# Kernel tuning notes

Measured on AMD Instinct MI355X. Metric: run time of the kernel, lower is better.

Reference implementation:

```python
import jax, jax.numpy as jnp
import numpy as np

N_AGENTS = 8192
OBS_DIM = 520
EMBED = 64
HID = 128
N_ACT = 6


def setup_inputs() -> dict:
    key = jax.random.key(0)
    ks = jax.random.split(key, 16)
    s = 0.05  # small init scale for numerical stability
    return {
        "obs": jax.random.normal(ks[0], (N_AGENTS, OBS_DIM), jnp.float32),
        "beliefs": jax.random.normal(ks[1], (N_AGENTS, HID), jnp.float32),
        "W1": jax.random.normal(ks[2], (OBS_DIM, EMBED), jnp.float32) * s,
        "b1": jnp.zeros((EMBED,), jnp.float32),
        "W2": jax.random.normal(ks[3], (EMBED, EMBED), jnp.float32) * s,
        "b2": jnp.zeros((EMBED,), jnp.float32),
        "Wb": jax.random.normal(ks[4], (HID, EMBED), jnp.float32) * s,
        "bb": jnp.zeros((EMBED,), jnp.float32),
        "Wg": jax.random.normal(ks[5], (2 * EMBED, HID), jnp.float32) * s,
        "bg": jnp.zeros((HID,), jnp.float32),
        "Wir": jax.random.normal(ks[6], (HID, HID), jnp.float32) * s,
        "Wiz": jax.random.normal(ks[7], (HID, HID), jnp.float32) * s,
        "Win": jax.random.normal(ks[8], (HID, HID), jnp.float32) * s,
        "Whr": jax.random.normal(ks[9], (HID, HID), jnp.float32) * s,
        "bhr": jnp.zeros((HID,), jnp.float32),
        "Whz": jax.random.normal(ks[10], (HID, HID), jnp.float32) * s,
        "bhz": jnp.zeros((HID,), jnp.float32),
        "Whn": jax.random.normal(ks[11], (HID, HID), jnp.float32) * s,
        "bhn": jnp.zeros((HID,), jnp.float32),
        "Wout": jax.random.normal(ks[12], (HID, N_ACT), jnp.float32) * s,
        "bout": jnp.zeros((N_ACT,), jnp.float32),
    }


def reference(obs, beliefs, W1, b1, W2, b2, Wb, bb, Wg, bg,
              Wir, Wiz, Win, Whr, bhr, Whz, bhz, Whn, bhn, Wout, bout):
    n_agents = obs.shape[0]
    # obs MLP: Dense -> relu -> Dense -> relu  [A, EMBED]
    h_obs = jax.nn.relu(obs @ W1 + b1)
    h_obs = jax.nn.relu(h_obs @ W2 + b2)
    # belief projection [A, EMBED]
    bp = beliefs @ Wb + bb
    # self-attention over beliefs with diagonal masked out
    attn_logits = (bp @ bp.T) / jnp.sqrt(jnp.asarray(EMBED, bp.dtype))
    attn_logits = attn_logits + jnp.eye(n_agents, dtype=bp.dtype) * (-1e8)
    attn_weights = jax.nn.softmax(attn_logits, axis=-1)
    contexts = attn_weights @ bp  # [A, EMBED]
    # GRU input projection [A, HID]
    gru_in = jnp.concatenate([h_obs, contexts], axis=-1) @ Wg + bg
    # flax GRUCell (input denses bias-free, hidden denses biased)
    r = jax.nn.sigmoid(gru_in @ Wir + beliefs @ Whr + bhr)
    z = jax.nn.sigmoid(gru_in @ Wiz + beliefs @ Whz + bhz)
    n = jnp.tanh(gru_in @ Win + r * (beliefs @ Whn + bhn))
    new_beliefs = (1.0 - z) * n + z * beliefs
    logits = new_beliefs @ Wout + bout
    return (logits, new_beliefs)
```

## Files before the change

### kernel.cpp

```cpp
#include <hip/hip_runtime.h>

#define A_N 8192
#define OBS_D 520
#define EMB 64
#define HID 128
#define NACT 6
#define SPLIT 16

typedef short bf16x8 __attribute__((ext_vector_type(8)));
typedef _Float16 half8 __attribute__((ext_vector_type(8)));
typedef float f32x4 __attribute__((ext_vector_type(4)));
typedef unsigned short u16;
typedef unsigned int u32;

#define MFMA_BF(a,b,c) __builtin_amdgcn_mfma_f32_16x16x32_bf16(a,b,c,0,0,0)
#define MFMA_FH(a,b,c) __builtin_amdgcn_mfma_f32_16x16x32_f16(a,b,c,0,0,0)

__device__ inline u32 fbits(float f){ union{float f; u32 u;}v; v.f=f; return v.u; }
__device__ inline float fval(u32 u){ union{u32 u; float f;}v; v.u=u; return v.f; }
__device__ inline u16 f2bf(float f){ u32 u=fbits(f); u += 0x7fffu + ((u>>16)&1u); return (u16)(u>>16); }
__device__ inline u32 pk_bf(float pe, float po){
  return __builtin_amdgcn_perm(fbits(po), fbits(pe), 0x07060302u);
}
__device__ inline float sigmoidf_fast(float x){
  x = fminf(fmaxf(x, -30.f), 30.f);
  return 1.f / (1.f + __expf(-x));
}
__device__ inline float tanhf_fast(float x){
  x = fminf(fmaxf(x, -15.f), 15.f);
  float e = __expf(-2.f*x);
  return (1.f - e) / (1.f + e);
}

#define EXP2C 0.18033688011112042f

__global__ __launch_bounds__(256) void kPrep(
    const float* __restrict__ Wg, const float* __restrict__ Wir,
    const float* __restrict__ Wiz, const float* __restrict__ Win,
    const float* __restrict__ Whr, const float* __restrict__ Whz,
    const float* __restrict__ Whn, const float* __restrict__ W1,
    const float* __restrict__ W2, const float* __restrict__ Wb,
    _Float16* __restrict__ WT, _Float16* __restrict__ W1T,
    _Float16* __restrict__ W2T, u16* __restrict__ WbT)
{
  __shared__ float tile[64][65];
  const int t = threadIdx.x, b = blockIdx.x;

  const float* src; int k0, c0, srcStride, kValid;
  if (b < 28) {
    const int mi = b >> 2, tl = b & 3;
    src = mi==0?Wg: mi==1?Wir: mi==2?Wiz: mi==3?Win: mi==4?Whr: mi==5?Whz: Whn;
    k0 = (tl >> 1) * 64; c0 = (tl & 1) * 64; srcStride = 128; kValid = 128;
  } else if (b < 37) {
    src = W1; k0 = (b - 28) * 64; c0 = 0; srcStride = 64; kValid = OBS_D;
  } else if (b < 38) {
    src = W2; k0 = 0; c0 = 0; srcStride = 64; kValid = 64;
  } else {
    src = Wb; k0 = (b - 38) * 64; c0 = 0; srcStride = 64; kValid = 128;
  }
  #pragma unroll
  for (int i = 0; i < 16; i++) {
    const int idx = i * 256 + t;
    const int rr = idx >> 6, cc = idx & 63;
    tile[rr][cc] = (k0 + rr < kValid) ? src[(size_t)(k0 + rr) * srcStride + c0 + cc] : 0.f;
  }
  __syncthreads();
  if (b < 28) {
    const int mi = b >> 2;
    _Float16* dst = WT + (size_t)mi * 16384;
    #pragma unroll
    for (int i = 0; i < 16; i++) {
      const int idx = i * 256 + t;
      const int rr = idx >> 6, cc = idx & 63;
      dst[(size_t)(c0 + rr) * 128 + k0 + cc] = (_Float16)tile[cc][rr];
    }
  } else if (b < 37) {
    #pragma unroll
    for (int i = 0; i < 16; i++) {
      const int idx = i * 256 + t;
      const int rr = idx >> 6, cc = idx & 63;
      if (k0 + cc < 544)
        W1T[(size_t)rr * 544 + k0 + cc] = (_Float16)tile[cc][rr];
    }
  } else if (b < 38) {
    #pragma unroll
    for (int i = 0; i < 16; i++) {
      const int idx = i * 256 + t;
      const int rr = idx >> 6, cc = idx & 63;
      W2T[(size_t)rr * 64 + cc] = (_Float16)tile[cc][rr];
    }
  } else {
    #pragma unroll
    for (int i = 0; i < 16; i++) {
      const int idx = i * 256 + t;
      const int rr = idx >> 6, cc = idx & 63;
      WbT[(size_t)rr * 128 + k0 + cc] = f2bf(tile[cc][rr]);
    }
  }
}

__global__ __launch_bounds__(256) void kA2(
    const float* __restrict__ beliefs, const u16* __restrict__ WbT,
    const float* __restrict__ bb, u16* __restrict__ bp, u16* __restrict__ bpT)
{
  const int lane = threadIdx.x & 63, wid = threadIdx.x >> 6;
  const int m = lane & 15, quad = lane >> 4;
  const int r0 = blockIdx.x * 64 + wid * 16;
  f32x4 c[4];
  #pragma unroll
  for (int ct = 0; ct < 4; ct++) c[ct] = (f32x4){0.f,0.f,0.f,0.f};

  #pragma unroll
  for (int s = 0; s < 4; s++) {
    const int k0 = s*32;
    const float* ap = beliefs + (size_t)(r0+m)*HID + k0 + quad*8;
    float4 a0 = *(const float4*)ap;
    float4 a1 = *(const float4*)(ap + 4);
    union { u16 e[8]; bf16x8 v; } av;
    av.e[0]=f2bf(a0.x); av.e[1]=f2bf(a0.y); av.e[2]=f2bf(a0.z); av.e[3]=f2bf(a0.w);
    av.e[4]=f2bf(a1.x); av.e[5]=f2bf(a1.y); av.e[6]=f2bf(a1.z); av.e[7]=f2bf(a1.w);
    #pragma unroll
    for (int ct = 0; ct < 4; ct++) {
      bf16x8 bw = *(const bf16x8*)(WbT + (size_t)(ct*16+m)*128 + k0 + quad*8);
      c[ct] = MFMA_BF(av.v, bw, c[ct]);
    }
  }
  #pragma unroll
  for (int ct = 0; ct < 4; ct++) {
    const int col = ct*16 + m;
    const float bbv = bb[col];
    u16 e[4];
    #pragma unroll
    for (int r = 0; r < 4; r++) e[r] = f2bf(c[ct][r] + bbv);
    #pragma unroll
    for (int r = 0; r < 4; r++)
      bp[(size_t)(r0 + quad*4 + r)*EMB + col] = e[r];
    uint2 pkv;
    pkv.x = (u32)e[0] | ((u32)e[1] << 16);
    pkv.y = (u32)e[2] | ((u32)e[3] << 16);
    *(uint2*)(bpT + (size_t)col*A_N + r0 + quad*4) = pkv;
  }
}

__global__ __launch_bounds__(256) void kM(
    const u16* __restrict__ bp, const u16* __restrict__ bpT,
    u16* __restrict__ ctxp, float* __restrict__ sums,
    const float* __restrict__ obs, const _Float16* __restrict__ W1T,
    const float* __restrict__ b1, const _Float16* __restrict__ W2T,
    const float* __restrict__ b2, _Float16* __restrict__ h2f)
{
  __shared__ __align__(16) u16 P[4][4][16 * 72];
  const int lane = threadIdx.x & 63;
  const int wid  = threadIdx.x >> 6;
  const int m = lane & 15, quad = lane >> 4;

  if (blockIdx.x >= 128) {
    const int w = (blockIdx.x - 128) * 4 + wid;
    const int split = w >> 7;
    const int qt = w & 127;
    const int q0 = qt * 64;

    bf16x8 qa[4][2];
    #pragma unroll
    for (int f = 0; f < 4; f++) {
      const u16* qr = bp + (size_t)(q0 + f*16 + m)*EMB + quad*8;
      qa[f][0] = *(const bf16x8*)(qr);
      qa[f][1] = *(const bf16x8*)(qr + 32);
    }
    f32x4 oacc[4][4];
    #pragma unroll
    for (int f = 0; f < 4; f++)
      #pragma unroll
      for (int d = 0; d < 4; d++) oacc[f][d] = (f32x4){0.f,0.f,0.f,0.f};
    float rowsum[4] = {0.f, 0.f, 0.f, 0.f};

    const int kbeg = split * (A_N / SPLIT);
    const int kend = kbeg + (A_N / SPLIT);

    for (int k0 = kbeg; k0 < kend; k0 += 64) {
      #pragma unroll
      for (int jt = 0; jt < 4; jt++) {
        const u16* kr = bp + (size_t)(k0 + jt*16 + m)*EMB + quad*8;
        const bf16x8 kb0 = *(const bf16x8*)(kr);
        const bf16x8 kb1 = *(const bf16x8*)(kr + 32);
        #pragma unroll
        for (int f = 0; f < 4; f++) {
          f32x4 s = (f32x4){0.f,0.f,0.f,0.f};
          s = MFMA_BF(kb0, qa[f][0], s);
          s = MFMA_BF(kb1, qa[f][1], s);
          float p0 = __builtin_amdgcn_exp2f(s[0]*EXP2C);
          float p1 = __builtin_amdgcn_exp2f(s[1]*EXP2C);
          float p2 = __builtin_amdgcn_exp2f(s[2]*EXP2C);
          float p3 = __builtin_amdgcn_exp2f(s[3]*EXP2C);
          if ((k0 + jt*16) == (q0 + f*16)) {
            const int jl = quad*4;
            if (jl + 0 == m) p0 = 0.f;
            if (jl + 1 == m) p1 = 0.f;
            if (jl + 2 == m) p2 = 0.f;
            if (jl + 3 == m) p3 = 0.f;
          }
          rowsum[f] += (p0 + p1) + (p2 + p3);
          uint2 pkv; pkv.x = pk_bf(p0, p1); pkv.y = pk_bf(p2, p3);
          *(uint2*)&P[wid][f][m*72 + jt*16 + quad*4] = pkv;
        }
      }
      bf16x8 vb[4][2];
      #pragma unroll
      for (int dtt = 0; dtt < 4; dtt++) {
        const u16* vr = bpT + (size_t)(dtt*16+m)*A_N + k0 + quad*8;
        vb[dtt][0] = *(const bf16x8*)(vr);
        vb[dtt][1] = *(const bf16x8*)(vr + 32);
      }
      asm volatile("s_waitcnt lgkmcnt(0)" ::: "memory");
      #pragma unroll
      for (int f = 0; f < 4; f++) {
        const bf16x8 pa0 = *(const bf16x8*)&P[wid][f][m*72 + quad*8];
        const bf16x8 pa1 = *(const bf16x8*)&P[wid][f][m*72 + 32 + quad*8];
        #pragma unroll
        for (int dtt = 0; dtt < 4; dtt++) {
          oacc[f][dtt] = MFMA_BF(pa0, vb[dtt][0], oacc[f][dtt]);
          oacc[f][dtt] = MFMA_BF(pa1, vb[dtt][1], oacc[f][dtt]);
        }
      }
    }

    #pragma unroll
    for (int f = 0; f < 4; f++) {
      float v = rowsum[f];
      v += __shfl_xor(v, 16, 64);
      v += __shfl_xor(v, 32, 64);
      if (lane < 16)
        sums[(size_t)split*A_N + q0 + f*16 + lane] = v;
    }
    #pragma unroll
    for (int f = 0; f < 4; f++) {
      const size_t base = ((size_t)split*A_N + q0 + f*16) * EMB;
      #pragma unroll
      for (int dtt = 0; dtt < 4; dtt++)
        #pragma unroll
        for (int r = 0; r < 4; r++)
          ctxp[base + (size_t)(quad*4+r)*EMB + dtt*16 + m] = f2bf(oacc[f][dtt][r]);
    }
  } else {
    const int r0 = blockIdx.x * 64 + wid * 16;
    f32x4 oa[4];
    #pragma unroll
    for (int ct = 0; ct < 4; ct++) oa[ct] = (f32x4){0.f,0.f,0.f,0.f};

    for (int s = 0; s < 17; s++) {
      const int k0 = s * 32;
      union { _Float16 e[8]; half8 v; } af;
      if (s < 16) {
        const float* ap = obs + (size_t)(r0+m)*OBS_D + k0 + quad*8;
        float4 a0 = *(const float4*)ap;
        float4 a1 = *(const float4*)(ap + 4);
        af.e[0]=(_Float16)a0.x; af.e[1]=(_Float16)a0.y; af.e[2]=(_Float16)a0.z; af.e[3]=(_Float16)a0.w;
        af.e[4]=(_Float16)a1.x; af.e[5]=(_Float16)a1.y; af.e[6]=(_Float16)a1.z; af.e[7]=(_Float16)a1.w;
      } else {
        #pragma unroll
        for (int j = 0; j < 8; j++) af.e[j] = (_Float16)0.f;
        if (quad == 0) {
          const float* ap = obs + (size_t)(r0+m)*OBS_D + 512;
          float4 a0 = *(const float4*)ap;
          float4 a1 = *(const float4*)(ap + 4);
          af.e[0]=(_Float16)a0.x; af.e[1]=(_Float16)a0.y; af.e[2]=(_Float16)a0.z; af.e[3]=(_Float16)a0.w;
          af.e[4]=(_Float16)a1.x; af.e[5]=(_Float16)a1.y; af.e[6]=(_Float16)a1.z; af.e[7]=(_Float16)a1.w;
        }
      }
      #pragma unroll
      for (int ct = 0; ct < 4; ct++) {
        half8 bw = *(const half8*)(W1T + (size_t)(ct*16+m)*544 + k0 + quad*8);
        oa[ct] = MFMA_FH(af.v, bw, oa[ct]);
      }
    }
    _Float16* H1 = (_Float16*)&P[wid][0][0];
    #pragma unroll
    for (int ct = 0; ct < 4; ct++) {
      const float b1v = b1[ct*16 + m];
      #pragma unroll
      for (int r = 0; r < 4; r++) {
        float v = fmaxf(oa[ct][r] + b1v, 0.f);
        H1[(quad*4+r)*72 + ct*16 + m] = (_Float16)v;
      }
    }
    __syncthreads();
    f32x4 ob[4];
    #pragma unroll
    for (int ct = 0; ct < 4; ct++) ob[ct] = (f32x4){0.f,0.f,0.f,0.f};
    #pragma unroll
    for (int s2 = 0; s2 < 2; s2++) {
      half8 ah = *(const half8*)(H1 + m*72 + s2*32 + quad*8);
      #pragma unroll
      for (int ct = 0; ct < 4; ct++) {
        half8 bw = *(const half8*)(W2T + (size_t)(ct*16+m)*64 + s2*32 + quad*8);
        ob[ct] = MFMA_FH(ah, bw, ob[ct]);
      }
    }
    #pragma unroll
    for (int ct = 0; ct < 4; ct++) {
      const float b2v = b2[ct*16 + m];
      #pragma unroll
      for (int r = 0; r < 4; r++) {
        float v = fmaxf(ob[ct][r] + b2v, 0.f);
        h2f[(size_t)(r0 + quad*4 + r)*EMB + ct*16 + m] = (_Float16)v;
      }
    }
  }
}

__global__ __launch_bounds__(256) void kRed(
    const u16* __restrict__ ctxp, const float* __restrict__ sums,
    _Float16* __restrict__ xh)
{
  const int idx = blockIdx.x * 256 + threadIdx.x;
  const int row = idx >> 5;
  const int cp  = idx & 31;
  float s0 = 0.f, s1 = 0.f, ss = 0.f;
  #pragma unroll
  for (int sp = 0; sp < SPLIT; sp++) {
    const u32 u = *(const u32*)(ctxp + ((size_t)sp*A_N + row)*EMB + cp*2);
    s0 += fval(u << 16);
    s1 += fval(u & 0xffff0000u);
    ss += sums[(size_t)sp*A_N + row];
  }
  const float inv = 1.f / ss;
  union { _Float16 e[2]; u32 u; } o;
  o.e[0] = (_Float16)(s0 * inv);
  o.e[1] = (_Float16)(s1 * inv);
  *(u32*)(xh + (size_t)row*EMB + cp*2) = o.u;
}

__global__ __launch_bounds__(256) void k3_gru(
    const float* __restrict__ beliefs, const _Float16* __restrict__ h2f,
    const _Float16* __restrict__ xh,
    const _Float16* __restrict__ WT,
    const float* __restrict__ bg, const float* __restrict__ bhr,
    const float* __restrict__ bhz, const float* __restrict__ bhn,
    const float* __restrict__ Wout, const float* __restrict__ bout,
    float* __restrict__ out)
{
  __shared__ _Float16 xf[16][136];
  __shared__ _Float16 belf[16][136];
  __shared__ _Float16 gruf[16][136];
  const int t = threadIdx.x;
  const int lane = t & 63, wid = t >> 6;
  const int m = lane & 15, quad = lane >> 4;
  const int r0 = blockIdx.x * 16;

  {
    const int row = t >> 4, seg = t & 15;
    const float* bpR = beliefs + (size_t)(r0+row)*HID + seg*8;
    float4 a0 = *(const float4*)bpR;
    float4 a1 = *(const float4*)(bpR + 4);
    union { _Float16 e[8]; half8 v; } hb;
    hb.e[0]=(_Float16)a0.x; hb.e[1]=(_Float16)a0.y; hb.e[2]=(_Float16)a0.z; hb.e[3]=(_Float16)a0.w;
    hb.e[4]=(_Float16)a1.x; hb.e[5]=(_Float16)a1.y; hb.e[6]=(_Float16)a1.z; hb.e[7]=(_Float16)a1.w;
    *(half8*)&belf[row][seg*8] = hb.v;
  }
  if (t < 128) {
    const int crow = t >> 3, cdg = t & 7;
    half8 hv = *(const half8*)(h2f + (size_t)(r0+crow)*EMB + cdg*8);
    *(half8*)&xf[crow][cdg*8] = hv;
    half8 xv = *(const half8*)(xh + (size_t)(r0+crow)*EMB + cdg*8);
    *(half8*)&xf[crow][64 + cdg*8] = xv;
  }
  __syncthreads();

  f32x4 g[2];
  g[0] = (f32x4){0.f,0.f,0.f,0.f}; g[1] = (f32x4){0.f,0.f,0.f,0.f};
  #pragma unroll
  for (int s = 0; s < 4; s++) {
    half8 ax = *(const half8*)&xf[m][s*32 + quad*8];
    #pragma unroll
    for (int ci = 0; ci < 2; ci++) {
      const int ct = wid*2 + ci;
      half8 bw = *(const half8*)(WT + (size_t)(ct*16+m)*128 + s*32 + quad*8);
      g[ci] = MFMA_FH(ax, bw, g[ci]);
    }
  }
  #pragma unroll
  for (int ci = 0; ci < 2; ci++) {
    const int col = (wid*2+ci)*16 + m;
    const float bgv = bg[col];
    #pragma unroll
    for (int r = 0; r < 4; r++)
      gruf[quad*4+r][col] = (_Float16)(g[ci][r] + bgv);
  }
  __syncthreads();

  f32x4 RV[2], ZV[2];
  #pragma unroll
  for (int gidx = 0; gidx < 3; gidx++) {
    const _Float16* WiTg = WT + (size_t)(1+gidx)*16384;
    const _Float16* WhTg = WT + (size_t)(4+gidx)*16384;
    f32x4 gi[2], gh[2];
    gi[0]=(f32x4){0.f,0.f,0.f,0.f}; gi[1]=(f32x4){0.f,0.f,0.f,0.f};
    gh[0]=(f32x4){0.f,0.f,0.f,0.f}; gh[1]=(f32x4){0.f,0.f,0.f,0.f};
    #pragma unroll
    for (int s = 0; s < 4; s++) {
      half8 ag = *(const half8*)&gruf[m][s*32 + quad*8];
      half8 ab = *(const half8*)&belf[m][s*32 + quad*8];
      #pragma unroll
      for (int ci = 0; ci < 2; ci++) {
        const int ct = wid*2 + ci;
        half8 bi = *(const half8*)(WiTg + (size_t)(ct*16+m)*128 + s*32 + quad*8);
        half8 bh = *(const half8*)(WhTg + (size_t)(ct*16+m)*128 + s*32 + quad*8);
        gi[ci] = MFMA_FH(ag, bi, gi[ci]);
        gh[ci] = MFMA_FH(ab, bh, gh[ci]);
      }
    }
    if (gidx == 0) {
      #pragma unroll
      for (int ci = 0; ci < 2; ci++) {
        const float bv = bhr[(wid*2+ci)*16 + m];
        #pragma unroll
        for (int r = 0; r < 4; r++) RV[ci][r] = sigmoidf_fast(gi[ci][r] + gh[ci][r] + bv);
      }
    } else if (gidx == 1) {
      #pragma unroll
      for (int ci = 0; ci < 2; ci++) {
        const float bv = bhz[(wid*2+ci)*16 + m];
        #pragma unroll
        for (int r = 0; r < 4; r++) ZV[ci][r] = sigmoidf_fast(gi[ci][r] + gh[ci][r] + bv);
      }
    } else {
      #pragma unroll
      for (int ci = 0; ci < 2; ci++) {
        const int col = (wid*2+ci)*16 + m;
        const float bv = bhn[col];
        #pragma unroll
        for (int r = 0; r < 4; r++) {
          const int row = quad*4 + r;
          float bel = beliefs[(size_t)(r0+row)*HID + col];
          float pre = gi[ci][r] + RV[ci][r] * (gh[ci][r] + bv);
          float nv = tanhf_fast(pre);
          float nb = (1.f - ZV[ci][r]) * nv + ZV[ci][r] * bel;
          out[(size_t)NACT*A_N + (size_t)(r0+row)*HID + col] = nb;
          xf[row][col] = (_Float16)nb;
        }
      }
    }
  }
  __syncthreads();

  if (t < 16*NACT) {
    const int row = t / NACT, c = t % NACT;
    float a = bout[c];
    #pragma unroll 8
    for (int k = 0; k < HID; k++)
      a += (float)xf[row][k] * Wout[(size_t)k*NACT + c];
    out[(size_t)(r0+row)*NACT + c] = a;
  }
}

extern "C" void kernel_launch(void* const* d_in, const int* in_sizes, int n_in,
                              void* d_out, int out_size, void* d_ws, size_t ws_size,
                              hipStream_t stream) {
  const float* obs     = (const float*)d_in[0];
  const float* beliefs = (const float*)d_in[1];
  const float* W1      = (const float*)d_in[2];
  const float* b1      = (const float*)d_in[3];
  const float* W2      = (const float*)d_in[4];
  const float* b2      = (const float*)d_in[5];
  const float* Wb      = (const float*)d_in[6];
  const float* bb      = (const float*)d_in[7];
  const float* Wg      = (const float*)d_in[8];
  const float* bg      = (const float*)d_in[9];
  const float* Wir     = (const float*)d_in[10];
  const float* Wiz     = (const float*)d_in[11];
  const float* Win     = (const float*)d_in[12];
  const float* Whr     = (const float*)d_in[13];
  const float* bhr     = (const float*)d_in[14];
  const float* Whz     = (const float*)d_in[15];
  const float* bhz     = (const float*)d_in[16];
  const float* Whn     = (const float*)d_in[17];
  const float* bhn     = (const float*)d_in[18];
  const float* Wout    = (const float*)d_in[19];
  const float* bout    = (const float*)d_in[20];
  float* out = (float*)d_out;

  char* ws = (char*)d_ws;
  _Float16* h2f  = (_Float16*)(ws);
  u16*      bp   = (u16*)(ws + 1048576);
  u16*      bpT  = (u16*)(ws + 2097152);
  u16*      ctxp = (u16*)(ws + 3145728);
  float*    sums = (float*)(ws + 19922944);
  _Float16* WT   = (_Float16*)(ws + 20447232);
  _Float16* W1T  = (_Float16*)(ws + 20676608);
  _Float16* W2T  = (_Float16*)(ws + 20746240);
  u16*      WbT  = (u16*)(ws + 20754432);
  _Float16* xh   = (_Float16*)(ws + 1048576);

  hipLaunchKernelGGL(kPrep, dim3(40), dim3(256), 0, stream,
                     Wg, Wir, Wiz, Win, Whr, Whz, Whn, W1, W2, Wb, WT, W1T, W2T, WbT);
  hipLaunchKernelGGL(kA2, dim3(128), dim3(256), 0, stream, beliefs, WbT, bb, bp, bpT);
  hipLaunchKernelGGL(kM, dim3(128 + (A_N / 64) * SPLIT / 4), dim3(256), 0, stream,
                     bp, bpT, ctxp, sums, obs, W1T, b1, W2T, b2, h2f);
  hipLaunchKernelGGL(kRed, dim3(1024), dim3(256), 0, stream, ctxp, sums, xh);
  hipLaunchKernelGGL(k3_gru, dim3(512), dim3(256), 0, stream,
                     beliefs, h2f, xh, WT, bg, bhr, bhz, bhn, Wout, bout, out);
}
```

Before: 187.4 us.

## Fuse belief projection into prep kernel, reorder kM blocks, double GRU rows per block

Merges the Wb transpose and belief projection kernel into the weight-prep kernel: each projection block converts Wb to bf16 in LDS itself, so one launch and the WbT global round trip go away. In kM the attention blocks now come first in the grid and the obs-MLP blocks after them, so the long attention work is scheduled earlier. The GRU kernel processes 32 rows per block instead of 16, reusing each loaded weight fragment for two MFMA row tiles and halving the grid. In exchange, every projection block redoes the Wb conversion, and the GRU kernel uses more LDS and registers with fewer blocks.

```diff
diff --git a/kernel.cpp b/kernel.cpp
--- a/kernel.cpp
+++ b/kernel.cpp
@@ -34,111 +34,111 @@
 
 #define EXP2C 0.18033688011112042f
 
-__global__ __launch_bounds__(256) void kPrep(
+__global__ __launch_bounds__(256) void kPrep2(
     const float* __restrict__ Wg, const float* __restrict__ Wir,
     const float* __restrict__ Wiz, const float* __restrict__ Win,
     const float* __restrict__ Whr, const float* __restrict__ Whz,
     const float* __restrict__ Whn, const float* __restrict__ W1,
     const float* __restrict__ W2, const float* __restrict__ Wb,
+    const float* __restrict__ beliefs, const float* __restrict__ bb,
     _Float16* __restrict__ WT, _Float16* __restrict__ W1T,
-    _Float16* __restrict__ W2T, u16* __restrict__ WbT)
+    _Float16* __restrict__ W2T, u16* __restrict__ bp, u16* __restrict__ bpT)
 {
   __shared__ float tile[64][65];
+  __shared__ u16 WbL[64][136];
   const int t = threadIdx.x, b = blockIdx.x;
 
-  const float* src; int k0, c0, srcStride, kValid;
-  if (b < 28) {
-    const int mi = b >> 2, tl = b & 3;
-    src = mi==0?Wg: mi==1?Wir: mi==2?Wiz: mi==3?Win: mi==4?Whr: mi==5?Whz: Whn;
-    k0 = (tl >> 1) * 64; c0 = (tl & 1) * 64; srcStride = 128; kValid = 128;
-  } else if (b < 37) {
-    src = W1; k0 = (b - 28) * 64; c0 = 0; srcStride = 64; kValid = OBS_D;
-  } else if (b < 38) {
-    src = W2; k0 = 0; c0 = 0; srcStride = 64; kValid = 64;
-  } else {
-    src = Wb; k0 = (b - 38) * 64; c0 = 0; srcStride = 64; kValid = 128;
-  }
-  #pragma unroll
-  for (int i = 0; i < 16; i++) {
-    const int idx = i * 256 + t;
-    const int rr = idx >> 6, cc = idx & 63;
-    tile[rr][cc] = (k0 + rr < kValid) ? src[(size_t)(k0 + rr) * srcStride + c0 + cc] : 0.f;
-  }
-  __syncthreads();
-  if (b < 28) {
-    const int mi = b >> 2;
-    _Float16* dst = WT + (size_t)mi * 16384;
+  if (b < 38) {
+    const float* src; int k0, c0, srcStride, kValid;
+    if (b < 28) {
+      const int mi = b >> 2, tl = b & 3;
+      src = mi==0?Wg: mi==1?Wir: mi==2?Wiz: mi==3?Win: mi==4?Whr: mi==5?Whz: Whn;
+      k0 = (tl >> 1) * 64; c0 = (tl & 1) * 64; srcStride = 128; kValid = 128;
+    } else if (b < 37) {
+      src = W1; k0 = (b - 28) * 64; c0 = 0; srcStride = 64; kValid = OBS_D;
+    } else {
+      src = W2; k0 = 0; c0 = 0; srcStride = 64; kValid = 64;
+    }
     #pragma unroll
     for (int i = 0; i < 16; i++) {
       const int idx = i * 256 + t;
       const int rr = idx >> 6, cc = idx & 63;
-      dst[(size_t)(c0 + rr) * 128 + k0 + cc] = (_Float16)tile[cc][rr];
-    }
-  } else if (b < 37) {
-    #pragma unroll
-    for (int i = 0; i < 16; i++) {
-      const int idx = i * 256 + t;
-      const int rr = idx >> 6, cc = idx & 63;
-      if (k0 + cc < 544)
-        W1T[(size_t)rr * 544 + k0 + cc] = (_Float16)tile[cc][rr];
-    }
-  } else if (b < 38) {
-    #pragma unroll
-    for (int i = 0; i < 16; i++) {
-      const int idx = i * 256 + t;
-      const int rr = idx >> 6, cc = idx & 63;
-      W2T[(size_t)rr * 64 + cc] = (_Float16)tile[cc][rr];
+      tile[rr][cc] = (k0 + rr < kValid) ? src[(size_t)(k0 + rr) * srcStride + c0 + cc] : 0.f;
+    }
+    __syncthreads();
+    if (b < 28) {
+      const int mi = b >> 2;
+      _Float16* dst = WT + (size_t)mi * 16384;
+      #pragma unroll
+      for (int i = 0; i < 16; i++) {
+        const int idx = i * 256 + t;
+        const int rr = idx >> 6, cc = idx & 63;
+        dst[(size_t)(c0 + rr) * 128 + k0 + cc] = (_Float16)tile[cc][rr];
+      }
+    } else if (b < 37) {
+      #pragma unroll
+      for (int i = 0; i < 16; i++) {
+        const int idx = i * 256 + t;
+        const int rr = idx >> 6, cc = idx & 63;
+        if (k0 + cc < 544)
+          W1T[(size_t)rr * 544 + k0 + cc] = (_Float16)tile[cc][rr];
+      }
+    } else {
+      #pragma unroll
+      for (int i = 0; i < 16; i++) {
+        const int idx = i * 256 + t;
+        const int rr = idx >> 6, cc = idx & 63;
+        W2T[(size_t)rr * 64 + cc] = (_Float16)tile[cc][rr];
+      }
     }
   } else {
-    #pragma unroll
-    for (int i = 0; i < 16; i++) {
-      const int idx = i * 256 + t;
-      const int rr = idx >> 6, cc = idx & 63;
-      WbT[(size_t)rr * 128 + k0 + cc] = f2bf(tile[cc][rr]);
-    }
-  }
-}
-
-__global__ __launch_bounds__(256) void kA2(
-    const float* __restrict__ beliefs, const u16* __restrict__ WbT,
-    const float* __restrict__ bb, u16* __restrict__ bp, u16* __restrict__ bpT)
-{
-  const int lane = threadIdx.x & 63, wid = threadIdx.x >> 6;
-  const int m = lane & 15, quad = lane >> 4;
-  const int r0 = blockIdx.x * 64 + wid * 16;
-  f32x4 c[4];
-  #pragma unroll
-  for (int ct = 0; ct < 4; ct++) c[ct] = (f32x4){0.f,0.f,0.f,0.f};
-
-  #pragma unroll
-  for (int s = 0; s < 4; s++) {
-    const int k0 = s*32;
-    const float* ap = beliefs + (size_t)(r0+m)*HID + k0 + quad*8;
-    float4 a0 = *(const float4*)ap;
-    float4 a1 = *(const float4*)(ap + 4);
-    union { u16 e[8]; bf16x8 v; } av;
-    av.e[0]=f2bf(a0.x); av.e[1]=f2bf(a0.y); av.e[2]=f2bf(a0.z); av.e[3]=f2bf(a0.w);
-    av.e[4]=f2bf(a1.x); av.e[5]=f2bf(a1.y); av.e[6]=f2bf(a1.z); av.e[7]=f2bf(a1.w);
+    const int lane = t & 63, wid = t >> 6;
+    const int m = lane & 15, quad = lane >> 4;
+    const int r0 = (b - 38) * 64 + wid * 16;
+
+    #pragma unroll
+    for (int i = 0; i < 8; i++) {
+      const int i4 = i * 256 + t;
+      float4 w4 = ((const float4*)Wb)[i4];
+      const int k = i4 >> 4, c = (i4 & 15) * 4;
+      WbL[c+0][k] = f2bf(w4.x); WbL[c+1][k] = f2bf(w4.y);
+      WbL[c+2][k] = f2bf(w4.z); WbL[c+3][k] = f2bf(w4.w);
+    }
+    __syncthreads();
+
+    f32x4 acc[4];
+    #pragma unroll
+    for (int ct = 0; ct < 4; ct++) acc[ct] = (f32x4){0.f,0.f,0.f,0.f};
+    #pragma unroll
+    for (int s = 0; s < 4; s++) {
+      const int k0 = s*32;
+      const float* ap = beliefs + (size_t)(r0+m)*HID + k0 + quad*8;
+      float4 a0 = *(const float4*)ap;
+      float4 a1 = *(const float4*)(ap + 4);
+      union { u16 e[8]; bf16x8 v; } av;
+      av.e[0]=f2bf(a0.x); av.e[1]=f2bf(a0.y); av.e[2]=f2bf(a0.z); av.e[3]=f2bf(a0.w);
+      av.e[4]=f2bf(a1.x); av.e[5]=f2bf(a1.y); av.e[6]=f2bf(a1.z); av.e[7]=f2bf(a1.w);
+      #pragma unroll
+      for (int ct = 0; ct < 4; ct++) {
+        bf16x8 bw = *(const bf16x8*)&WbL[ct*16+m][k0 + quad*8];
+        acc[ct] = MFMA_BF(av.v, bw, acc[ct]);
+      }
+    }
     #pragma unroll
     for (int ct = 0; ct < 4; ct++) {
-      bf16x8 bw = *(const bf16x8*)(WbT + (size_t)(ct*16+m)*128 + k0 + quad*8);
-      c[ct] = MFMA_BF(av.v, bw, c[ct]);
-    }
-  }
-  #pragma unroll
-  for (int ct = 0; ct < 4; ct++) {
-    const int col = ct*16 + m;
-    const float bbv = bb[col];
-    u16 e[4];
-    #pragma unroll
-    for (int r = 0; r < 4; r++) e[r] = f2bf(c[ct][r] + bbv);
-    #pragma unroll
-    for (int r = 0; r < 4; r++)
-      bp[(size_t)(r0 + quad*4 + r)*EMB + col] = e[r];
-    uint2 pkv;
-    pkv.x = (u32)e[0] | ((u32)e[1] << 16);
-    pkv.y = (u32)e[2] | ((u32)e[3] << 16);
-    *(uint2*)(bpT + (size_t)col*A_N + r0 + quad*4) = pkv;
+      const int col = ct*16 + m;
+      const float bbv = bb[col];
+      u16 e[4];
+      #pragma unroll
+      for (int r = 0; r < 4; r++) e[r] = f2bf(acc[ct][r] + bbv);
+      #pragma unroll
+      for (int r = 0; r < 4; r++)
+        bp[(size_t)(r0 + quad*4 + r)*EMB + col] = e[r];
+      uint2 pkv;
+      pkv.x = (u32)e[0] | ((u32)e[1] << 16);
+      pkv.y = (u32)e[2] | ((u32)e[3] << 16);
+      *(uint2*)(bpT + (size_t)col*A_N + r0 + quad*4) = pkv;
+    }
   }
 }
 
@@ -154,8 +154,8 @@
   const int wid  = threadIdx.x >> 6;
   const int m = lane & 15, quad = lane >> 4;
 
-  if (blockIdx.x >= 128) {
-    const int w = (blockIdx.x - 128) * 4 + wid;
+  if (blockIdx.x < 512) {
+    const int w = blockIdx.x * 4 + wid;
     const int split = w >> 7;
     const int qt = w & 127;
     const int q0 = qt * 64;
@@ -242,7 +242,7 @@
           ctxp[base + (size_t)(quad*4+r)*EMB + dtt*16 + m] = f2bf(oacc[f][dtt][r]);
     }
   } else {
-    const int r0 = blockIdx.x * 64 + wid * 16;
+    const int r0 = (blockIdx.x - 512) * 64 + wid * 16;
     f32x4 oa[4];
     #pragma unroll
     for (int ct = 0; ct < 4; ct++) oa[ct] = (f32x4){0.f,0.f,0.f,0.f};
@@ -339,16 +339,18 @@
     const float* __restrict__ Wout, const float* __restrict__ bout,
     float* __restrict__ out)
 {
-  __shared__ _Float16 xf[16][136];
-  __shared__ _Float16 belf[16][136];
-  __shared__ _Float16 gruf[16][136];
+  __shared__ _Float16 xf[32][136];
+  __shared__ _Float16 belf[32][136];
+  __shared__ _Float16 gruf[32][136];
   const int t = threadIdx.x;
   const int lane = t & 63, wid = t >> 6;
   const int m = lane & 15, quad = lane >> 4;
-  const int r0 = blockIdx.x * 16;
-
-  {
-    const int row = t >> 4, seg = t & 15;
+  const int r0 = blockIdx.x * 32;
+
+  #pragma unroll
+  for (int i = 0; i < 2; i++) {
+    const int idx = i*256 + t;
+    const int row = idx >> 4, seg = idx & 15;
     const float* bpR = beliefs + (size_t)(r0+row)*HID + seg*8;
     float4 a0 = *(const float4*)bpR;
     float4 a1 = *(const float4*)(bpR + 4);
@@ -357,93 +359,120 @@
     hb.e[4]=(_Float16)a1.x; hb.e[5]=(_Float16)a1.y; hb.e[6]=(_Float16)a1.z; hb.e[7]=(_Float16)a1.w;
     *(half8*)&belf[row][seg*8] = hb.v;
   }
-  if (t < 128) {
-    const int crow = t >> 3, cdg = t & 7;
-    half8 hv = *(const half8*)(h2f + (size_t)(r0+crow)*EMB + cdg*8);
-    *(half8*)&xf[crow][cdg*8] = hv;
-    half8 xv = *(const half8*)(xh + (size_t)(r0+crow)*EMB + cdg*8);
-    *(half8*)&xf[crow][64 + cdg*8] = xv;
+  #pragma unroll
+  for (int i = 0; i < 2; i++) {
+    const int idx = i*256 + t;
+    const int row = idx >> 4, seg = idx & 15;
+    if (seg < 8) {
+      half8 hv = *(const half8*)(h2f + (size_t)(r0+row)*EMB + seg*8);
+      *(half8*)&xf[row][seg*8] = hv;
+    } else {
+      half8 xv = *(const half8*)(xh + (size_t)(r0+row)*EMB + (seg-8)*8);
+      *(half8*)&xf[row][64 + (seg-8)*8] = xv;
+    }
   }
   __syncthreads();
 
-  f32x4 g[2];
-  g[0] = (f32x4){0.f,0.f,0.f,0.f}; g[1] = (f32x4){0.f,0.f,0.f,0.f};
+  f32x4 g[2][2];
+  #pragma unroll
+  for (int rt = 0; rt < 2; rt++)
+    #pragma unroll
+    for (int ci = 0; ci < 2; ci++) g[rt][ci] = (f32x4){0.f,0.f,0.f,0.f};
   #pragma unroll
   for (int s = 0; s < 4; s++) {
-    half8 ax = *(const half8*)&xf[m][s*32 + quad*8];
+    half8 bw0 = *(const half8*)(WT + (size_t)((wid*2+0)*16+m)*128 + s*32 + quad*8);
+    half8 bw1 = *(const half8*)(WT + (size_t)((wid*2+1)*16+m)*128 + s*32 + quad*8);
+    #pragma unroll
+    for (int rt = 0; rt < 2; rt++) {
+      half8 ax = *(const half8*)&xf[rt*16 + m][s*32 + quad*8];
+      g[rt][0] = MFMA_FH(ax, bw0, g[rt][0]);
+      g[rt][1] = MFMA_FH(ax, bw1, g[rt][1]);
+    }
+  }
+  #pragma unroll
+  for (int rt = 0; rt < 2; rt++)
     #pragma unroll
     for (int ci = 0; ci < 2; ci++) {
-      const int ct = wid*2 + ci;
-      half8 bw = *(const half8*)(WT + (size_t)(ct*16+m)*128 + s*32 + quad*8);
-      g[ci] = MFMA_FH(ax, bw, g[ci]);
-    }
-  }
-  #pragma unroll
-  for (int ci = 0; ci < 2; ci++) {
-    const int col = (wid*2+ci)*16 + m;
-    const float bgv = bg[col];
-    #pragma unroll
-    for (int r = 0; r < 4; r++)
-      gruf[quad*4+r][col] = (_Float16)(g[ci][r] + bgv);
-  }
+      const int col = (wid*2+ci)*16 + m;
+      const float bgv = bg[col];
+      #pragma unroll
+      for (int r = 0; r < 4; r++)
+        gruf[rt*16 + quad*4 + r][col] = (_Float16)(g[rt][ci][r] + bgv);
+    }
   __syncthreads();
 
-  f32x4 RV[2], ZV[2];
+  f32x4 RV[2][2], ZV[2][2];
   #pragma unroll
   for (int gidx = 0; gidx < 3; gidx++) {
     const _Float16* WiTg = WT + (size_t)(1+gidx)*16384;
     const _Float16* WhTg = WT + (size_t)(4+gidx)*16384;
-    f32x4 gi[2], gh[2];
-    gi[0]=(f32x4){0.f,0.f,0.f,0.f}; gi[1]=(f32x4){0.f,0.f,0.f,0.f};
-    gh[0]=(f32x4){0.f,0.f,0.f,0.f}; gh[1]=(f32x4){0.f,0.f,0.f,0.f};
+    f32x4 gi[2][2], gh[2][2];
+    #pragma unroll
+    for (int rt = 0; rt < 2; rt++)
+      #pragma unroll
+      for (int ci = 0; ci < 2; ci++) {
+        gi[rt][ci] = (f32x4){0.f,0.f,0.f,0.f};
+        gh[rt][ci] = (f32x4){0.f,0.f,0.f,0.f};
+      }
     #pragma unroll
     for (int s = 0; s < 4; s++) {
-      half8 ag = *(const half8*)&gruf[m][s*32 + quad*8];
-      half8 ab = *(const half8*)&belf[m][s*32 + quad*8];
-      #pragma unroll
-      for (int ci = 0; ci < 2; ci++) {
-        const int ct = wid*2 + ci;
-        half8 bi = *(const half8*)(WiTg + (size_t)(ct*16+m)*128 + s*32 + quad*8);
-        half8 bh = *(const half8*)(WhTg + (size_t)(ct*16+m)*128 + s*32 + quad*8);
-        gi[ci] = MFMA_FH(ag, bi, gi[ci]);
-        gh[ci] = MFMA_FH(ab, bh, gh[ci]);
+      half8 bi0 = *(const half8*)(WiTg + (size_t)((wid*2+0)*16+m)*128 + s*32 + quad*8);
+      half8 bi1 = *(const half8*)(WiTg + (size_t)((wid*2+1)*16+m)*128 + s*32 + quad*8);
+      half8 bh0 = *(const half8*)(WhTg + (size_t)((wid*2+0)*16+m)*128 + s*32 + quad*8);
+      half8 bh1 = *(const half8*)(WhTg + (size_t)((wid*2+1)*16+m)*128 + s*32 + quad*8);
+      #pragma unroll
+      for (int rt = 0; rt < 2; rt++) {
+        half8 ag = *(const half8*)&gruf[rt*16 + m][s*32 + quad*8];
+        half8 ab = *(const half8*)&belf[rt*16 + m][s*32 + quad*8];
+        gi[rt][0] = MFMA_FH(ag, bi0, gi[rt][0]);
+        gi[rt][1] = MFMA_FH(ag, bi1, gi[rt][1]);
+        gh[rt][0] = MFMA_FH(ab, bh0, gh[rt][0]);
+        gh[rt][1] = MFMA_FH(ab, bh1, gh[rt][1]);
       }
     }
     if (gidx == 0) {
       #pragma unroll
-      for (int ci = 0; ci < 2; ci++) {
-        const float bv = bhr[(wid*2+ci)*16 + m];
-        #pragma unroll
-        for (int r = 0; r < 4; r++) RV[ci][r] = sigmoidf_fast(gi[ci][r] + gh[ci][r] + bv);
-      }
+      for (int rt = 0; rt < 2; rt++)
+        #pragma unroll
+        for (int ci = 0; ci < 2; ci++) {
+          const float bv = bhr[(wid*2+ci)*16 + m];
+          #pragma unroll
+          for (int r = 0; r < 4; r++)
+            RV[rt][ci][r] = sigmoidf_fast(gi[rt][ci][r] + gh[rt][ci][r] + bv);
+        }
     } else if (gidx == 1) {
       #pragma unroll
-      for (int ci = 0; ci < 2; ci++) {
-        const float bv = bhz[(wid*2+ci)*16 + m];
-        #pragma unroll
-        for (int r = 0; r < 4; r++) ZV[ci][r] = sigmoidf_fast(gi[ci][r] + gh[ci][r] + bv);
-      }
+      for (int rt = 0; rt < 2; rt++)
+        #pragma unroll
+        for (int ci = 0; ci < 2; ci++) {
+          const float bv = bhz[(wid*2+ci)*16 + m];
+          #pragma unroll
+          for (int r = 0; r < 4; r++)
+            ZV[rt][ci][r] = sigmoidf_fast(gi[rt][ci][r] + gh[rt][ci][r] + bv);
+        }
     } else {
       #pragma unroll
-      for (int ci = 0; ci < 2; ci++) {
-        const int col = (wid*2+ci)*16 + m;
-        const float bv = bhn[col];
-        #pragma unroll
-        for (int r = 0; r < 4; r++) {
-          const int row = quad*4 + r;
-          float bel = beliefs[(size_t)(r0+row)*HID + col];
-          float pre = gi[ci][r] + RV[ci][r] * (gh[ci][r] + bv);
-          float nv = tanhf_fast(pre);
-          float nb = (1.f - ZV[ci][r]) * nv + ZV[ci][r] * bel;
-          out[(size_t)NACT*A_N + (size_t)(r0+row)*HID + col] = nb;
-          xf[row][col] = (_Float16)nb;
+      for (int rt = 0; rt < 2; rt++)
+        #pragma unroll
+        for (int ci = 0; ci < 2; ci++) {
+          const int col = (wid*2+ci)*16 + m;
+          const float bv = bhn[col];
+          #pragma unroll
+          for (int r = 0; r < 4; r++) {
+            const int row = rt*16 + quad*4 + r;
+            float bel = beliefs[(size_t)(r0+row)*HID + col];
+            float pre = gi[rt][ci][r] + RV[rt][ci][r] * (gh[rt][ci][r] + bv);
+            float nv = tanhf_fast(pre);
+            float nb = (1.f - ZV[rt][ci][r]) * nv + ZV[rt][ci][r] * bel;
+            out[(size_t)NACT*A_N + (size_t)(r0+row)*HID + col] = nb;
+            xf[row][col] = (_Float16)nb;
+          }
         }
-      }
     }
   }
   __syncthreads();
 
-  if (t < 16*NACT) {
+  if (t < 32*NACT) {
     const int row = t / NACT, c = t % NACT;
     float a = bout[c];
     #pragma unroll 8
@@ -488,15 +517,14 @@
   _Float16* WT   = (_Float16*)(ws + 20447232);
   _Float16* W1T  = (_Float16*)(ws + 20676608);
   _Float16* W2T  = (_Float16*)(ws + 20746240);
-  u16*      WbT  = (u16*)(ws + 20754432);
   _Float16* xh   = (_Float16*)(ws + 1048576);
 
-  hipLaunchKernelGGL(kPrep, dim3(40), dim3(256), 0, stream,
-                     Wg, Wir, Wiz, Win, Whr, Whz, Whn, W1, W2, Wb, WT, W1T, W2T, WbT);
-  hipLaunchKernelGGL(kA2, dim3(128), dim3(256), 0, stream, beliefs, WbT, bb, bp, bpT);
-  hipLaunchKernelGGL(kM, dim3(128 + (A_N / 64) * SPLIT / 4), dim3(256), 0, stream,
+  hipLaunchKernelGGL(kPrep2, dim3(166), dim3(256), 0, stream,
+                     Wg, Wir, Wiz, Win, Whr, Whz, Whn, W1, W2, Wb, beliefs, bb,
+                     WT, W1T, W2T, bp, bpT);
+  hipLaunchKernelGGL(kM, dim3(640), dim3(256), 0, stream,
                      bp, bpT, ctxp, sums, obs, W1T, b1, W2T, b2, h2f);
   hipLaunchKernelGGL(kRed, dim3(1024), dim3(256), 0, stream, ctxp, sums, xh);
-  hipLaunchKernelGGL(k3_gru, dim3(512), dim3(256), 0, stream,
+  hipLaunchKernelGGL(k3_gru, dim3(256), dim3(256), 0, stream,
                      beliefs, h2f, xh, WT, bg, bhr, bhz, bhn, Wout, bout, out);
 }
```

Result: faster. 176.9 us (-5.6%).
